# Kernel optimization log

Measured on AMD Instinct MI355X. Metric: run time of the kernel, lower is better.

Reference implementation:

```python
import jax, jax.numpy as jnp
import numpy as np

DIM = 512
N_PATCH = 1024
HEADS = 8
LN_EPS = 1e-5
NORM_EPS = 1e-12


def _layernorm(x, g, b):
    mu = jnp.mean(x, axis=-1, keepdims=True)
    var = jnp.mean(jnp.square(x - mu), axis=-1, keepdims=True)
    return (x - mu) * jax.lax.rsqrt(var + LN_EPS) * g + b


def _l2norm(x):
    # matches F.normalize(dim=-1): x / max(||x||, eps)
    n = jnp.sqrt(jnp.sum(jnp.square(x), axis=-1, keepdims=True))
    return x / jnp.maximum(n, NORM_EPS)


def _gelu(x):
    return jax.nn.gelu(x, approximate=False)


def _cosine_attn_branch(x, qkv_w, qkv_b, ln_g, ln_b, proj_w, proj_b, temperature):
    B, N, D = x.shape
    H = HEADS
    hd = D // H
    qkv = _layernorm(x @ qkv_w + qkv_b, ln_g, ln_b)          # [B,N,3D]
    q, k, v = jnp.split(qkv, 3, axis=-1)
    def to_heads(t):
        return t.reshape(B, N, H, hd).transpose(0, 2, 1, 3)  # [B,H,N,hd]
    q, k, v = to_heads(q), to_heads(k), to_heads(v)
    q = _l2norm(q)
    k = _l2norm(k)
    # temperature: [H,1,1] broadcasts over [B,H,N,N]
    attn = jnp.einsum('bhnd,bhmd->bhnm', q, k) * temperature
    attn = jax.nn.softmax(attn, axis=-1)
    out = jnp.einsum('bhnm,bhmd->bhnd', attn, v)
    out = out.transpose(0, 2, 1, 3).reshape(B, N, D)
    return out @ proj_w + proj_b


def setup_inputs() -> dict:
    key = jax.random.key(0)
    ks = iter(jax.random.split(key, 40))
    D = DIM
    def rn(shape, scale=0.02):
        return (jax.random.normal(next(ks), shape, dtype=jnp.float32) * scale)
    inp = {
        'hsi_tokens': jax.random.normal(next(ks), (8, N_PATCH, D), dtype=jnp.float32),
        'lidar_tokens': jax.random.normal(next(ks), (8, N_PATCH, D), dtype=jnp.float32),
        'temperature': jnp.ones((HEADS, 1, 1), dtype=jnp.float32),
        'sq_w': rn((D, 3 * D)), 'sq_b': jnp.zeros((3 * D,), jnp.float32),
        'sq_ln_g': jnp.ones((3 * D,), jnp.float32), 'sq_ln_b': jnp.zeros((3 * D,), jnp.float32),
        'sproj_w': rn((D, D)), 'sproj_b': jnp.zeros((D,), jnp.float32),
        'pq_w': rn((D, 3 * D)), 'pq_b': jnp.zeros((3 * D,), jnp.float32),
        'pq_ln_g': jnp.ones((3 * D,), jnp.float32), 'pq_ln_b': jnp.zeros((3 * D,), jnp.float32),
        'pproj_w': rn((D, D)), 'pproj_b': jnp.zeros((D,), jnp.float32),
        'vf_w1': rn((D, 2 * D)), 'vf_b1': jnp.zeros((2 * D,), jnp.float32),
        'vf_w2': rn((2 * D, D)), 'vf_b2': jnp.zeros((D,), jnp.float32),
        'ag_w1': rn((2 * D, D)), 'ag_b1': jnp.zeros((D,), jnp.float32),
        'ag_ln_g': jnp.ones((D,), jnp.float32), 'ag_ln_b': jnp.zeros((D,), jnp.float32),
        'ag_w2': rn((D, 3)), 'ag_b2': jnp.zeros((3,), jnp.float32),
        'fr_w1': rn((D, 2 * D)), 'fr_b1': jnp.zeros((2 * D,), jnp.float32),
        'fr_w2': rn((2 * D, D)), 'fr_b2': jnp.zeros((D,), jnp.float32),
        'alpha': jnp.ones((1,), jnp.float32),
        'beta': jnp.ones((1,), jnp.float32),
    }
    return inp


def reference(hsi_tokens, lidar_tokens, temperature,
              sq_w, sq_b, sq_ln_g, sq_ln_b, sproj_w, sproj_b,
              pq_w, pq_b, pq_ln_g, pq_ln_b, pproj_w, pproj_b,
              vf_w1, vf_b1, vf_w2, vf_b2,
              ag_w1, ag_b1, ag_ln_g, ag_ln_b, ag_w2, ag_b2,
              fr_w1, fr_b1, fr_w2, fr_b2, alpha, beta):
    B, N, D = hsi_tokens.shape
    out_spectral = _cosine_attn_branch(hsi_tokens, sq_w, sq_b, sq_ln_g, sq_ln_b,
                                       sproj_w, sproj_b, temperature)
    out_spatial = _cosine_attn_branch(lidar_tokens, pq_w, pq_b, pq_ln_g, pq_ln_b,
                                      pproj_w, pproj_b, temperature)
    # volumetric fusion MLP (dropout is identity in eval)
    s = out_spectral + out_spatial
    volumetric_feat = _gelu(s @ vf_w1 + vf_b1) @ vf_w2 + vf_b2
    # adaptive gating
    hsi_global = jnp.mean(out_spectral, axis=1)    # [B,D]
    lidar_global = jnp.mean(out_spatial, axis=1)   # [B,D]
    concat = jnp.concatenate([hsi_global, lidar_global], axis=-1)  # [B,2D]
    g = _gelu(_layernorm(concat @ ag_w1 + ag_b1, ag_ln_g, ag_ln_b))
    gate = jax.nn.softmax(g @ ag_w2 + ag_b2, axis=-1)  # [B,3]
    w_spec = gate[:, 0][:, None, None]
    w_spat = gate[:, 1][:, None, None]
    w_vol = gate[:, 2][:, None, None]
    fused = w_spec * out_spectral + w_spat * out_spatial + w_vol * volumetric_feat
    fused_recal = _gelu(fused @ fr_w1 + fr_b1) @ fr_w2 + fr_b2
    return fused + alpha * fused_recal + beta * (hsi_tokens + lidar_tokens) * 0.5
```

## Files before the change

kernel.cpp:

```cpp
#include <hip/hip_runtime.h>
#include <hip/hip_bf16.h>
#include <math.h>

#define B_   8
#define N_   1024
#define D_   512
#define H_   8
#define HD_  64
#define D3_  1536
#define M_   (B_ * N_)

#define WOFF_SQ    0
#define WOFF_PQ    786432
#define WOFF_SPROJ 1572864
#define WOFF_PPROJ 1835008
#define WOFF_VF1   2097152
#define WOFF_VF2   2621440
#define WOFF_FR1   3145728
#define WOFF_FR2   3670016

typedef float f32x4 __attribute__((ext_vector_type(4)));
typedef __bf16 bf16x8 __attribute__((ext_vector_type(8)));

union FragU {
    uint4 u4;
    unsigned int u[4];
    ushort s[8];
    bf16x8 v;
};

static __device__ __forceinline__ ushort f2bf(float x) {
    union { __bf16 h; ushort u; } c;
    c.h = (__bf16)x;
    return c.u;
}

static __device__ __forceinline__ float bf2f(ushort u) {
    union { unsigned u; float f; } c;
    c.u = ((unsigned)u) << 16;
    return c.f;
}

static __device__ __forceinline__ unsigned int pack2(float a, float b) {
    return (unsigned int)f2bf(a) | ((unsigned int)f2bf(b) << 16);
}

static __device__ __forceinline__ float gelu_f(float x) {
    return 0.5f * x * (1.0f + erff(x * 0.7071067811865475f));
}

#if __has_builtin(__builtin_amdgcn_exp2f)
static __device__ __forceinline__ float exp2_fast(float x) { return __builtin_amdgcn_exp2f(x); }
#else
static __device__ __forceinline__ float exp2_fast(float x) { return exp2f(x); }
#endif

static __device__ __forceinline__ void gload16(const ushort* g, ushort* lds) {
    __builtin_amdgcn_global_load_lds(
        (const __attribute__((address_space(1))) void*)g,
        (__attribute__((address_space(3))) void*)lds, 16, 0, 0);
}

static __device__ __forceinline__ float blk_sum(float v, float* red) {
    #pragma unroll
    for (int off = 32; off; off >>= 1) v += __shfl_xor(v, off);
    const int w = threadIdx.x >> 6;
    __syncthreads();
    if ((threadIdx.x & 63) == 0) red[w] = v;
    __syncthreads();
    return red[0] + red[1] + red[2] + red[3];
}

template <int BM, int BN, int ACT, int OUT, bool FINAL, bool GROUP>
__global__ __launch_bounds__(256) void pgemm_k(
    const ushort* __restrict__ A, const ushort* __restrict__ Wt,
    const ushort* __restrict__ Wt2, const float* __restrict__ bias,
    const float* __restrict__ bias2, int Msplit,
    void* __restrict__ Cv, int nbx, int Nn, int K,
    const ushort* __restrict__ fusedb, const float* __restrict__ r1,
    const float* __restrict__ r2, const float* __restrict__ alphap,
    const float* __restrict__ betap)
{
    constexpr int MI = BM / 32;
    constexpr int NJ = BN / 32;
    constexpr int CA = BM / 16;
    constexpr int CB = BN / 16;
    __shared__ ushort Asm[2][BM * 32];
    __shared__ ushort Bsm[2][BN * 32];
    const int tid = threadIdx.x;
    const int w = tid >> 6, l = tid & 63;
    const int cpx = gridDim.x >> 3;
    const int wg = (blockIdx.x & 7) * cpx + (blockIdx.x >> 3);
    const int m0 = (wg / nbx) * BM, n0 = (wg % nbx) * BN;
    const int wr = w >> 1, wc = w & 1;
    const int lr = l & 15, g = l >> 4;

    const ushort* W_ = (!GROUP || m0 < Msplit) ? Wt : Wt2;
    const float* b_ = (!GROUP || m0 < Msplit) ? bias : bias2;

    f32x4 acc[MI][NJ] = {};
    const int nt = K >> 5;

    #define STAGE(buf, kt)                                                        \
        do {                                                                      \
            const int k0s = (kt) << 5;                                            \
            for (int c = w; c < CA; c += 4)                                       \
                gload16(&A[(size_t)(m0 + c * 16 + lr) * K + k0s + 8 * g],         \
                        &Asm[buf][c * 512]);                                      \
            for (int c = w; c < CB; c += 4)                                       \
                gload16(&W_[(size_t)(n0 + c * 16 + lr) * K + k0s + 8 * g],        \
                        &Bsm[buf][c * 512]);                                      \
        } while (0)

    STAGE(0, 0);
    __syncthreads();
    int cur = 0;
    for (int t = 0; t < nt; ++t) {
        if (t + 1 < nt) STAGE(cur ^ 1, t + 1);
        FragU af[MI], bf4[NJ];
        #pragma unroll
        for (int mi = 0; mi < MI; ++mi)
            af[mi].u4 = *reinterpret_cast<const uint4*>(
                &Asm[cur][(wr * MI + mi) * 512 + l * 8]);
        #pragma unroll
        for (int nj = 0; nj < NJ; ++nj)
            bf4[nj].u4 = *reinterpret_cast<const uint4*>(
                &Bsm[cur][(wc * NJ + nj) * 512 + l * 8]);
        #pragma unroll
        for (int mi = 0; mi < MI; ++mi)
            #pragma unroll
            for (int nj = 0; nj < NJ; ++nj)
                acc[mi][nj] = __builtin_amdgcn_mfma_f32_16x16x32_bf16(
                    af[mi].v, bf4[nj].v, acc[mi][nj], 0, 0, 0);
        __syncthreads();
        cur ^= 1;
    }
    #undef STAGE

    float alpha = 0.f, beta = 0.f;
    if (FINAL) { alpha = alphap[0]; beta = betap[0]; }
    #pragma unroll
    for (int mi = 0; mi < MI; ++mi) {
        #pragma unroll
        for (int r = 0; r < 4; ++r) {
            const int m = m0 + wr * (MI * 16) + mi * 16 + g * 4 + r;
            #pragma unroll
            for (int nj = 0; nj < NJ; ++nj) {
                const int n = n0 + wc * (NJ * 16) + nj * 16 + lr;
                const size_t idx = (size_t)m * Nn + n;
                float v = acc[mi][nj][r] + b_[n];
                if (ACT == 1) v = gelu_f(v);
                if (FINAL)
                    v = bf2f(fusedb[idx]) + alpha * v + 0.5f * beta * (r1[idx] + r2[idx]);
                if (OUT == 0) ((float*)Cv)[idx] = v;
                else          ((ushort*)Cv)[idx] = f2bf(v);
            }
        }
    }
}

__global__ __launch_bounds__(256) void cvtw_k(
    const float* __restrict__ w0, const float* __restrict__ w1,
    const float* __restrict__ w2, const float* __restrict__ w3,
    const float* __restrict__ w4, const float* __restrict__ w5,
    const float* __restrict__ w6, const float* __restrict__ w7,
    ushort* __restrict__ dst)
{
    __shared__ ushort T[64][72];
    const int id = blockIdx.z;
    int K, Nn, off;
    const float* src;
    switch (id) {
        case 0: src = w0; K = 512;  Nn = 1536; off = WOFF_SQ;    break;
        case 1: src = w1; K = 512;  Nn = 1536; off = WOFF_PQ;    break;
        case 2: src = w2; K = 512;  Nn = 512;  off = WOFF_SPROJ; break;
        case 3: src = w3; K = 512;  Nn = 512;  off = WOFF_PPROJ; break;
        case 4: src = w4; K = 512;  Nn = 1024; off = WOFF_VF1;   break;
        case 5: src = w5; K = 1024; Nn = 512;  off = WOFF_VF2;   break;
        case 6: src = w6; K = 512;  Nn = 1024; off = WOFF_FR1;   break;
        default: src = w7; K = 1024; Nn = 512; off = WOFF_FR2;   break;
    }
    const int n0 = blockIdx.x * 64, k0 = blockIdx.y * 64;
    if (n0 >= Nn || k0 >= K) return;
    const int t = threadIdx.x;
    const int q = t >> 6, e = t & 63;
    #pragma unroll 4
    for (int i = 0; i < 16; ++i) {
        const int kl = q * 16 + i;
        T[e][kl] = f2bf(src[(size_t)(k0 + kl) * Nn + n0 + e]);
    }
    __syncthreads();
    #pragma unroll 4
    for (int i = 0; i < 16; ++i) {
        const int nl = q * 16 + i;
        dst[(size_t)off + (size_t)(n0 + nl) * K + k0 + e] = T[nl][e];
    }
}

__global__ __launch_bounds__(256) void cvt_k(const float* __restrict__ a,
                                             ushort* __restrict__ dst)
{
    const size_t i = ((size_t)blockIdx.x * 256 + threadIdx.x) * 8;
    const float4 x0 = *reinterpret_cast<const float4*>(a + i);
    const float4 x1 = *reinterpret_cast<const float4*>(a + i + 4);
    FragU o;
    o.u[0] = pack2(x0.x, x0.y);
    o.u[1] = pack2(x0.z, x0.w);
    o.u[2] = pack2(x1.x, x1.y);
    o.u[3] = pack2(x1.z, x1.w);
    *reinterpret_cast<uint4*>(dst + i) = o.u4;
}

__global__ __launch_bounds__(256) void cvtadd_k(const ushort* __restrict__ a,
                                                const ushort* __restrict__ b,
                                                ushort* __restrict__ dst)
{
    const size_t i = ((size_t)blockIdx.x * 256 + threadIdx.x) * 8;
    FragU x, y, o;
    x.u4 = *reinterpret_cast<const uint4*>(a + i);
    y.u4 = *reinterpret_cast<const uint4*>(b + i);
    #pragma unroll
    for (int e = 0; e < 8; ++e) o.s[e] = f2bf(bf2f(x.s[e]) + bf2f(y.s[e]));
    *reinterpret_cast<uint4*>(dst + i) = o.u4;
}

__global__ __launch_bounds__(256) void lnprep_k(ushort* __restrict__ x,
                                                const float* __restrict__ lng0,
                                                const float* __restrict__ lnb0,
                                                const float* __restrict__ lng1,
                                                const float* __restrict__ lnb1,
                                                const float* __restrict__ temp,
                                                ushort* __restrict__ Kb,
                                                ushort* __restrict__ Vt)
{
    __shared__ ushort Vs[8 * 512];
    const int w = threadIdx.x >> 6, l = threadIdx.x & 63;
    const int n0 = blockIdx.x * 8;
    const float L2E = 1.4426950408889634f;
    const float* lng = (n0 < 8192) ? lng0 : lng1;
    const float* lnb = (n0 < 8192) ? lnb0 : lnb1;

    #pragma unroll
    for (int rr = 0; rr < 2; ++rr) {
        const int row = n0 + w * 2 + rr;
        const int bb = row >> 10;
        const int n = row & 1023;
        ushort* xr = x + (size_t)row * D3_;
        float qv[24];
        #pragma unroll
        for (int i = 0; i < 24; ++i) qv[i] = bf2f(xr[l + 64 * i]);
        float s = 0.f, ss = 0.f;
        #pragma unroll
        for (int i = 0; i < 24; ++i) { s += qv[i]; ss += qv[i] * qv[i]; }
        #pragma unroll
        for (int off = 32; off; off >>= 1) {
            s += __shfl_xor(s, off);
            ss += __shfl_xor(ss, off);
        }
        const float mu = s * (1.0f / D3_);
        const float var = ss * (1.0f / D3_) - mu * mu;
        const float rs = rsqrtf(var + 1e-5f);
        #pragma unroll
        for (int i = 0; i < 24; ++i)
            qv[i] = (qv[i] - mu) * rs * lng[l + 64 * i] + lnb[l + 64 * i];
        float sq[16];
        #pragma unroll
        for (int i = 0; i < 16; ++i) sq[i] = qv[i] * qv[i];
        #pragma unroll
        for (int off = 32; off; off >>= 1)
            #pragma unroll
            for (int i = 0; i < 16; ++i) sq[i] += __shfl_xor(sq[i], off);
        #pragma unroll
        for (int i = 0; i < 8; ++i) {
            const float qs = temp[i] * L2E / fmaxf(sqrtf(sq[i]), 1e-12f);
            xr[i * 64 + l] = f2bf(qv[i] * qs);
        }
        #pragma unroll
        for (int i = 0; i < 8; ++i) {
            const float ks = 1.0f / fmaxf(sqrtf(sq[8 + i]), 1e-12f);
            Kb[((size_t)(bb * 8 + i) * N_ + n) * HD_ + l] = f2bf(qv[8 + i] * ks);
        }
        #pragma unroll
        for (int i = 0; i < 8; ++i)
            Vs[(w * 2 + rr) * 512 + i * 64 + l] = f2bf(qv[16 + i]);
    }
    __syncthreads();
    const int bb = n0 >> 10;
    #pragma unroll
    for (int it = 0; it < 2; ++it) {
        const int combo = threadIdx.x + it * 256;
        FragU f;
        #pragma unroll
        for (int tok = 0; tok < 8; ++tok) f.s[tok] = Vs[tok * 512 + combo];
        *reinterpret_cast<uint4*>(
            &Vt[((size_t)(bb * 8 + (combo >> 6)) * HD_ + (combo & 63)) * N_ + (n0 & 1023)]) = f.u4;
    }
}

__global__ __launch_bounds__(256) void fattn_k(const ushort* __restrict__ Qu,
                                               const ushort* __restrict__ Kb,
                                               const ushort* __restrict__ Vt,
                                               const float* __restrict__ temp,
                                               ushort* __restrict__ out)
{
    __shared__ ushort Ks[64 * 72];
    __shared__ ushort Vs[64 * 72];
    const int tid = threadIdx.x;
    const int cpx = gridDim.x >> 3;
    const int wg = (blockIdx.x & 7) * cpx + (blockIdx.x >> 3);
    const int nb = wg & 7;
    const int h  = (wg >> 3) & 7;
    const int bb = wg >> 6;
    const int bh = bb * 8 + h;
    const int n0 = nb * 128;
    const int w  = tid >> 6;
    const int l  = tid & 63;
    const int lr = l & 15;
    const int g  = l >> 4;
    const float m2 = fabsf(temp[h]) * 1.4426950408889634f;

    const int qb = n0 + w * 32;
    FragU qa0, qa1, qb0, qb1;
    {
        const size_t rb0 = (size_t)(bb * N_ + qb + lr) * D3_ + h * 64 + 8 * g;
        const size_t rb1 = (size_t)(bb * N_ + qb + 16 + lr) * D3_ + h * 64 + 8 * g;
        qa0.u4 = *reinterpret_cast<const uint4*>(&Qu[rb0]);
        qa1.u4 = *reinterpret_cast<const uint4*>(&Qu[rb0 + 32]);
        qb0.u4 = *reinterpret_cast<const uint4*>(&Qu[rb1]);
        qb1.u4 = *reinterpret_cast<const uint4*>(&Qu[rb1 + 32]);
    }

    f32x4 OA[4] = {};
    f32x4 OB[4] = {};
    float lsA = 0.f, lsB = 0.f;

    const ushort* kbase = Kb + (size_t)bh * N_ * HD_;
    const ushort* vbase = Vt + (size_t)bh * HD_ * N_;
    const int sr = tid >> 3;
    const int sc = (tid & 7) * 8;
    uint4 k0r, k1r, v0r, v1r;

    #define LOADT(kt)                                                           \
        do {                                                                    \
            const ushort* ks_ = kbase + (size_t)((kt) * 64) * HD_;              \
            const ushort* vs_ = vbase + (kt) * 64;                              \
            k0r = *reinterpret_cast<const uint4*>(ks_ + sr * HD_ + sc);         \
            k1r = *reinterpret_cast<const uint4*>(ks_ + (sr + 32) * HD_ + sc);  \
            v0r = *reinterpret_cast<const uint4*>(vs_ + (size_t)sr * N_ + sc);  \
            v1r = *reinterpret_cast<const uint4*>(vs_ + (size_t)(sr + 32) * N_ + sc); \
        } while (0)
    #define WRITET()                                                            \
        do {                                                                    \
            *reinterpret_cast<uint4*>(&Ks[sr * 72 + sc]) = k0r;                 \
            *reinterpret_cast<uint4*>(&Ks[(sr + 32) * 72 + sc]) = k1r;          \
            *reinterpret_cast<uint4*>(&Vs[sr * 72 + sc]) = v0r;                 \
            *reinterpret_cast<uint4*>(&Vs[(sr + 32) * 72 + sc]) = v1r;          \
        } while (0)

    LOADT(0);
    WRITET();
    __syncthreads();

    #pragma unroll 1
    for (int kt = 0; kt < 16; ++kt) {
        if (kt < 15) LOADT(kt + 1);

        unsigned paA[2][4], paB[2][4];
        #pragma unroll
        for (int j = 0; j < 4; ++j) {
            FragU ka, kc;
            ka.u4 = *reinterpret_cast<const uint4*>(&Ks[(j * 16 + lr) * 72 + 8 * g]);
            kc.u4 = *reinterpret_cast<const uint4*>(&Ks[(j * 16 + lr) * 72 + 32 + 8 * g]);
            f32x4 sA = {0.f,0.f,0.f,0.f}, sB = {0.f,0.f,0.f,0.f};
            sA = __builtin_amdgcn_mfma_f32_16x16x32_bf16(ka.v, qa0.v, sA, 0, 0, 0);
            sA = __builtin_amdgcn_mfma_f32_16x16x32_bf16(kc.v, qa1.v, sA, 0, 0, 0);
            sB = __builtin_amdgcn_mfma_f32_16x16x32_bf16(ka.v, qb0.v, sB, 0, 0, 0);
            sB = __builtin_amdgcn_mfma_f32_16x16x32_bf16(kc.v, qb1.v, sB, 0, 0, 0);
            float pA[4], pB[4];
            #pragma unroll
            for (int r = 0; r < 4; ++r) {
                pA[r] = exp2_fast(sA[r] - m2);
                pB[r] = exp2_fast(sB[r] - m2);
                lsA += pA[r];
                lsB += pB[r];
            }
            paA[j >> 1][2 * (j & 1) + 0] = pack2(pA[0], pA[1]);
            paA[j >> 1][2 * (j & 1) + 1] = pack2(pA[2], pA[3]);
            paB[j >> 1][2 * (j & 1) + 0] = pack2(pB[0], pB[1]);
            paB[j >> 1][2 * (j & 1) + 1] = pack2(pB[2], pB[3]);
        }

        #pragma unroll
        for (int ks = 0; ks < 2; ++ks) {
            FragU fa, fb2;
            fa.u[0] = paA[ks][0]; fa.u[1] = paA[ks][1];
            fa.u[2] = paA[ks][2]; fa.u[3] = paA[ks][3];
            fb2.u[0] = paB[ks][0]; fb2.u[1] = paB[ks][1];
            fb2.u[2] = paB[ks][2]; fb2.u[3] = paB[ks][3];
            #pragma unroll
            for (int s4 = 0; s4 < 4; ++s4) {
                FragU vb;
                const int vi = (lr + 16 * s4) * 72 + ks * 32 + 4 * g;
                *reinterpret_cast<uint2*>(&vb.u[0]) =
                    *reinterpret_cast<const uint2*>(&Vs[vi]);
                *reinterpret_cast<uint2*>(&vb.u[2]) =
                    *reinterpret_cast<const uint2*>(&Vs[vi + 16]);
                OA[s4] = __builtin_amdgcn_mfma_f32_16x16x32_bf16(fa.v, vb.v, OA[s4], 0, 0, 0);
                OB[s4] = __builtin_amdgcn_mfma_f32_16x16x32_bf16(fb2.v, vb.v, OB[s4], 0, 0, 0);
            }
        }

        if (kt < 15) {
            __syncthreads();
            WRITET();
            __syncthreads();
        }
    }
    #undef LOADT
    #undef WRITET

    lsA += __shfl_xor(lsA, 16); lsA += __shfl_xor(lsA, 32);
    lsB += __shfl_xor(lsB, 16); lsB += __shfl_xor(lsB, 32);
    const float invA = 1.0f / lsA;
    const float invB = 1.0f / lsB;
    ushort* outp = out + ((size_t)(bb * N_) + qb) * D_ + h * HD_;
    #pragma unroll
    for (int r = 0; r < 4; ++r) {
        const float iA = __shfl(invA, 4 * g + r);
        const float iB = __shfl(invB, 4 * g + r);
        ushort* rowA = outp + (size_t)(4 * g + r) * D_;
        ushort* rowB = outp + (size_t)(16 + 4 * g + r) * D_;
        #pragma unroll
        for (int s4 = 0; s4 < 4; ++s4) {
            rowA[s4 * 16 + lr] = f2bf(OA[s4][r] * iA);
            rowB[s4 * 16 + lr] = f2bf(OB[s4][r] * iB);
        }
    }
}

__global__ __launch_bounds__(256) void means_k(const ushort* __restrict__ spec,
                                               const ushort* __restrict__ spat,
                                               float* __restrict__ Gp)
{
    const int b = blockIdx.x >> 5;
    const int ch = blockIdx.x & 31;
    const int n0 = ch * 32;
    const int d0 = threadIdx.x * 2;
    float s1a = 0.f, s1b = 0.f, s2a = 0.f, s2b = 0.f;
    #pragma unroll 4
    for (int n = 0; n < 32; ++n) {
        const size_t idx = ((size_t)(b * N_) + n0 + n) * D_ + d0;
        ushort u1[2], u2[2];
        *reinterpret_cast<unsigned*>(u1) = *reinterpret_cast<const unsigned*>(spec + idx);
        *reinterpret_cast<unsigned*>(u2) = *reinterpret_cast<const unsigned*>(spat + idx);
        s1a += bf2f(u1[0]); s1b += bf2f(u1[1]);
        s2a += bf2f(u2[0]); s2b += bf2f(u2[1]);
    }
    float* gp = Gp + (size_t)blockIdx.x * 1024;
    gp[d0] = s1a; gp[d0 + 1] = s1b;
    gp[512 + d0] = s2a; gp[512 + d0 + 1] = s2b;
}

__global__ __launch_bounds__(256) void gate1_k(const float* __restrict__ Gp,
                                               const float* __restrict__ w1,
                                               const float* __restrict__ b1,
                                               float* __restrict__ y)
{
    __shared__ float xs[1024];
    __shared__ float red[4][64];
    const int jc = blockIdx.x, b = blockIdx.y, tid = threadIdx.x;
    for (int k = tid; k < 1024; k += 256) {
        float s = 0.f;
        #pragma unroll 8
        for (int c = 0; c < 32; ++c) s += Gp[(size_t)(b * 32 + c) * 1024 + k];
        xs[k] = s * (1.0f / N_);
    }
    __syncthreads();
    const int jl = tid & 63;
    const int jj = jc * 64 + jl;
    const int seg = tid >> 6;
    float acc = 0.f;
    const float* wp = w1 + (size_t)(seg * 256) * 512 + jj;
    const float* xp = xs + seg * 256;
    #pragma unroll 8
    for (int k = 0; k < 256; ++k) acc += xp[k] * wp[(size_t)k * 512];
    red[seg][jl] = acc;
    __syncthreads();
    if (tid < 64)
        y[b * 512 + jc * 64 + tid] =
            red[0][tid] + red[1][tid] + red[2][tid] + red[3][tid] + b1[jc * 64 + tid];
}

__global__ __launch_bounds__(256) void gate2_k(const float* __restrict__ y,
                                               const float* __restrict__ lng,
                                               const float* __restrict__ lnb,
                                               const float* __restrict__ w2,
                                               const float* __restrict__ b2,
                                               float* __restrict__ gate)
{
    __shared__ float red[4];
    const int b = blockIdx.x, tid = threadIdx.x;
    const float v0 = y[b * 512 + tid];
    const float v1 = y[b * 512 + 256 + tid];
    const float s = blk_sum(v0 + v1, red);
    const float ss = blk_sum(v0 * v0 + v1 * v1, red);
    const float mu = s * (1.0f / 512.0f);
    const float var = ss * (1.0f / 512.0f) - mu * mu;
    const float rs = rsqrtf(var + 1e-5f);
    const float z0 = gelu_f((v0 - mu) * rs * lng[tid] + lnb[tid]);
    const float z1 = gelu_f((v1 - mu) * rs * lng[tid + 256] + lnb[tid + 256]);
    float p0 = z0 * w2[tid * 3 + 0] + z1 * w2[(tid + 256) * 3 + 0];
    float p1 = z0 * w2[tid * 3 + 1] + z1 * w2[(tid + 256) * 3 + 1];
    float p2 = z0 * w2[tid * 3 + 2] + z1 * w2[(tid + 256) * 3 + 2];
    p0 = blk_sum(p0, red);
    p1 = blk_sum(p1, red);
    p2 = blk_sum(p2, red);
    if (tid == 0) {
        p0 += b2[0]; p1 += b2[1]; p2 += b2[2];
        const float m = fmaxf(p0, fmaxf(p1, p2));
        const float e0 = expf(p0 - m), e1 = expf(p1 - m), e2 = expf(p2 - m);
        const float inv = 1.0f / (e0 + e1 + e2);
        gate[b * 3 + 0] = e0 * inv;
        gate[b * 3 + 1] = e1 * inv;
        gate[b * 3 + 2] = e2 * inv;
    }
}

__global__ __launch_bounds__(256) void fuse_k(
    const ushort* __restrict__ spec, const ushort* __restrict__ spat,
    const ushort* __restrict__ volb, const float* __restrict__ gate,
    ushort* __restrict__ fb)
{
    const size_t i4 = ((size_t)blockIdx.x * 256 + threadIdx.x) * 4;
    const int b = (int)(i4 >> 19);
    const float g0 = gate[b * 3 + 0], g1 = gate[b * 3 + 1], g2 = gate[b * 3 + 2];
    ushort au[4], cu[4], vu[4];
    *reinterpret_cast<uint2*>(au) = *reinterpret_cast<const uint2*>(spec + i4);
    *reinterpret_cast<uint2*>(cu) = *reinterpret_cast<const uint2*>(spat + i4);
    *reinterpret_cast<uint2*>(vu) = *reinterpret_cast<const uint2*>(volb + i4);
    union { ushort s[4]; uint2 u; } ob;
    #pragma unroll
    for (int e = 0; e < 4; ++e)
        ob.s[e] = f2bf(g0 * bf2f(au[e]) + g1 * bf2f(cu[e]) + g2 * bf2f(vu[e]));
    *reinterpret_cast<uint2*>(fb + i4) = ob.u;
}

extern "C" void kernel_launch(void* const* d_in, const int* in_sizes, int n_in,
                              void* d_out, int out_size, void* d_ws, size_t ws_size,
                              hipStream_t stream)
{
    const float* hsi    = (const float*)d_in[0];
    const float* lidar  = (const float*)d_in[1];
    const float* temp   = (const float*)d_in[2];
    const float* sq_w   = (const float*)d_in[3];
    const float* sq_b   = (const float*)d_in[4];
    const float* sq_lng = (const float*)d_in[5];
    const float* sq_lnb = (const float*)d_in[6];
    const float* sproj_w = (const float*)d_in[7];
    const float* sproj_b = (const float*)d_in[8];
    const float* pq_w   = (const float*)d_in[9];
    const float* pq_b   = (const float*)d_in[10];
    const float* pq_lng = (const float*)d_in[11];
    const float* pq_lnb = (const float*)d_in[12];
    const float* pproj_w = (const float*)d_in[13];
    const float* pproj_b = (const float*)d_in[14];
    const float* vf_w1  = (const float*)d_in[15];
    const float* vf_b1  = (const float*)d_in[16];
    const float* vf_w2  = (const float*)d_in[17];
    const float* vf_b2  = (const float*)d_in[18];
    const float* ag_w1  = (const float*)d_in[19];
    const float* ag_b1  = (const float*)d_in[20];
    const float* ag_lng = (const float*)d_in[21];
    const float* ag_lnb = (const float*)d_in[22];
    const float* ag_w2  = (const float*)d_in[23];
    const float* ag_b2  = (const float*)d_in[24];
    const float* fr_w1  = (const float*)d_in[25];
    const float* fr_b1  = (const float*)d_in[26];
    const float* fr_w2  = (const float*)d_in[27];
    const float* fr_b2  = (const float*)d_in[28];
    const float* alpha  = (const float*)d_in[29];
    const float* beta   = (const float*)d_in[30];
    float* out = (float*)d_out;

    ushort* base = (ushort*)d_ws;
    ushort* Qkv  = base;
    ushort* Ob   = base;
    ushort* Sb   = base + 8388608;
    ushort* volb = base + 12582912;
    ushort* fb   = base + 16777216;
    float*  Gp   = (float*)(base + 20971520);
    float*  gate = Gp + 262144;
    float*  ybuf = gate + 64;
    ushort* Kb   = base + 25165824;
    ushort* Vt   = base + 33554432;
    ushort* Hb   = base + 25165824;
    ushort* Ab   = base + 41943040;
    ushort* Xb   = base + 41943040;
    ushort* Wb   = base + 50331648;

    const dim3 blk(256);

    cvtw_k<<<dim3(24, 16, 8), blk, 0, stream>>>(sq_w, pq_w, sproj_w, pproj_w,
                                                vf_w1, vf_w2, fr_w1, fr_w2, Wb);
    cvt_k<<<2048, blk, 0, stream>>>(hsi, Xb);
    cvt_k<<<2048, blk, 0, stream>>>(lidar, Xb + (size_t)M_ * D_);

    pgemm_k<128,128,0,1,false,true><<<1536, blk, 0, stream>>>(
        Xb, Wb + WOFF_SQ, Wb + WOFF_PQ, sq_b, pq_b, M_,
        Qkv, 12, D3_, D_, nullptr, nullptr, nullptr, nullptr, nullptr);

    lnprep_k<<<2048, blk, 0, stream>>>(Qkv, sq_lng, sq_lnb, pq_lng, pq_lnb,
                                       temp, Kb, Vt);

    fattn_k<<<1024, blk, 0, stream>>>(Qkv, Kb, Vt, temp, Ab);

    pgemm_k<128,64,0,1,false,true><<<1024, blk, 0, stream>>>(
        Ab, Wb + WOFF_SPROJ, Wb + WOFF_PPROJ, sproj_b, pproj_b, M_,
        Ob, 8, D_, D_, nullptr, nullptr, nullptr, nullptr, nullptr);

    const ushort* spec_b = Ob;
    const ushort* spat_b = Ob + (size_t)M_ * D_;

    means_k<<<256, blk, 0, stream>>>(spec_b, spat_b, Gp);
    gate1_k<<<dim3(8, 8), blk, 0, stream>>>(Gp, ag_w1, ag_b1, ybuf);
    gate2_k<<<B_, blk, 0, stream>>>(ybuf, ag_lng, ag_lnb, ag_w2, ag_b2, gate);

    cvtadd_k<<<2048, blk, 0, stream>>>(spec_b, spat_b, Sb);
    pgemm_k<128,64,1,1,false,false><<<1024, blk, 0, stream>>>(
        Sb, Wb + WOFF_VF1, nullptr, vf_b1, nullptr, 0,
        Hb, 16, 1024, D_, nullptr, nullptr, nullptr, nullptr, nullptr);
    pgemm_k<128,64,0,1,false,false><<<512, blk, 0, stream>>>(
        Hb, Wb + WOFF_VF2, nullptr, vf_b2, nullptr, 0,
        volb, 8, D_, 1024, nullptr, nullptr, nullptr, nullptr, nullptr);

    fuse_k<<<4096, blk, 0, stream>>>(spec_b, spat_b, volb, gate, fb);
    pgemm_k<128,64,1,1,false,false><<<1024, blk, 0, stream>>>(
        fb, Wb + WOFF_FR1, nullptr, fr_b1, nullptr, 0,
        Hb, 16, 1024, D_, nullptr, nullptr, nullptr, nullptr, nullptr);
    pgemm_k<128,64,0,0,true,false><<<512, blk, 0, stream>>>(
        Hb, Wb + WOFF_FR2, nullptr, fr_b2, nullptr, 0,
        out, 8, D_, 1024, fb, hsi, lidar, alpha, beta);
}
```

Measured before the change: 355.3 us.

## Fuse input conversions with bf16 residual and move softmax sums onto MFMA

Merges the two input conversion kernels into one that also writes a bf16 half-sum residual, so the final GEMM epilogue reads one bf16 array instead of two fp32 inputs. In flash attention, the max offset is folded into the MFMA accumulator init, row sums are computed with an MFMA against a ones vector instead of scalar adds and shuffles, and V shared-memory stores and loads are XOR-swizzled to reduce bank conflicts. The residual now carries bf16 rounding, and the row sums use the bf16-rounded probabilities rather than the fp32 values.

```diff
diff --git a/kernel.cpp b/kernel.cpp
--- a/kernel.cpp
+++ b/kernel.cpp
@@ -77,9 +77,8 @@
     const ushort* __restrict__ Wt2, const float* __restrict__ bias,
     const float* __restrict__ bias2, int Msplit,
     void* __restrict__ Cv, int nbx, int Nn, int K,
-    const ushort* __restrict__ fusedb, const float* __restrict__ r1,
-    const float* __restrict__ r2, const float* __restrict__ alphap,
-    const float* __restrict__ betap)
+    const ushort* __restrict__ fusedb, const ushort* __restrict__ resb,
+    const float* __restrict__ alphap, const float* __restrict__ betap)
 {
     constexpr int MI = BM / 32;
     constexpr int NJ = BN / 32;
@@ -151,7 +150,7 @@
                 float v = acc[mi][nj][r] + b_[n];
                 if (ACT == 1) v = gelu_f(v);
                 if (FINAL)
-                    v = bf2f(fusedb[idx]) + alpha * v + 0.5f * beta * (r1[idx] + r2[idx]);
+                    v = bf2f(fusedb[idx]) + alpha * v + beta * bf2f(resb[idx]);
                 if (OUT == 0) ((float*)Cv)[idx] = v;
                 else          ((ushort*)Cv)[idx] = f2bf(v);
             }
@@ -197,18 +196,29 @@
     }
 }
 
-__global__ __launch_bounds__(256) void cvt_k(const float* __restrict__ a,
-                                             ushort* __restrict__ dst)
+__global__ __launch_bounds__(256) void cvt3_k(const float* __restrict__ h,
+                                              const float* __restrict__ l,
+                                              ushort* __restrict__ xh,
+                                              ushort* __restrict__ xl,
+                                              ushort* __restrict__ rb)
 {
     const size_t i = ((size_t)blockIdx.x * 256 + threadIdx.x) * 8;
-    const float4 x0 = *reinterpret_cast<const float4*>(a + i);
-    const float4 x1 = *reinterpret_cast<const float4*>(a + i + 4);
-    FragU o;
-    o.u[0] = pack2(x0.x, x0.y);
-    o.u[1] = pack2(x0.z, x0.w);
-    o.u[2] = pack2(x1.x, x1.y);
-    o.u[3] = pack2(x1.z, x1.w);
-    *reinterpret_cast<uint4*>(dst + i) = o.u4;
+    const float4 h0 = *reinterpret_cast<const float4*>(h + i);
+    const float4 h1 = *reinterpret_cast<const float4*>(h + i + 4);
+    const float4 l0 = *reinterpret_cast<const float4*>(l + i);
+    const float4 l1 = *reinterpret_cast<const float4*>(l + i + 4);
+    FragU oh, ol, orr;
+    oh.u[0] = pack2(h0.x, h0.y); oh.u[1] = pack2(h0.z, h0.w);
+    oh.u[2] = pack2(h1.x, h1.y); oh.u[3] = pack2(h1.z, h1.w);
+    ol.u[0] = pack2(l0.x, l0.y); ol.u[1] = pack2(l0.z, l0.w);
+    ol.u[2] = pack2(l1.x, l1.y); ol.u[3] = pack2(l1.z, l1.w);
+    orr.u[0] = pack2(0.5f * (h0.x + l0.x), 0.5f * (h0.y + l0.y));
+    orr.u[1] = pack2(0.5f * (h0.z + l0.z), 0.5f * (h0.w + l0.w));
+    orr.u[2] = pack2(0.5f * (h1.x + l1.x), 0.5f * (h1.y + l1.y));
+    orr.u[3] = pack2(0.5f * (h1.z + l1.z), 0.5f * (h1.w + l1.w));
+    *reinterpret_cast<uint4*>(xh + i) = oh.u4;
+    *reinterpret_cast<uint4*>(xl + i) = ol.u4;
+    *reinterpret_cast<uint4*>(rb + i) = orr.u4;
 }
 
 __global__ __launch_bounds__(256) void cvtadd_k(const ushort* __restrict__ a,
@@ -318,6 +328,10 @@
     const int lr = l & 15;
     const int g  = l >> 4;
     const float m2 = fabsf(temp[h]) * 1.4426950408889634f;
+    const f32x4 mInit = {-m2, -m2, -m2, -m2};
+
+    FragU ones;
+    ones.u[0] = ones.u[1] = ones.u[2] = ones.u[3] = 0x3F803F80u;
 
     const int qb = n0 + w * 32;
     FragU qa0, qa1, qb0, qb1;
@@ -332,12 +346,14 @@
 
     f32x4 OA[4] = {};
     f32x4 OB[4] = {};
-    float lsA = 0.f, lsB = 0.f;
+    f32x4 LSA = {0.f, 0.f, 0.f, 0.f};
+    f32x4 LSB = {0.f, 0.f, 0.f, 0.f};
 
     const ushort* kbase = Kb + (size_t)bh * N_ * HD_;
     const ushort* vbase = Vt + (size_t)bh * HD_ * N_;
     const int sr = tid >> 3;
     const int sc = (tid & 7) * 8;
+    const int scv = sc ^ (8 * (sr & 1));
     uint4 k0r, k1r, v0r, v1r;
 
     #define LOADT(kt)                                                           \
@@ -353,8 +369,8 @@
         do {                                                                    \
             *reinterpret_cast<uint4*>(&Ks[sr * 72 + sc]) = k0r;                 \
             *reinterpret_cast<uint4*>(&Ks[(sr + 32) * 72 + sc]) = k1r;          \
-            *reinterpret_cast<uint4*>(&Vs[sr * 72 + sc]) = v0r;                 \
-            *reinterpret_cast<uint4*>(&Vs[(sr + 32) * 72 + sc]) = v1r;          \
+            *reinterpret_cast<uint4*>(&Vs[sr * 72 + scv]) = v0r;                \
+            *reinterpret_cast<uint4*>(&Vs[(sr + 32) * 72 + scv]) = v1r;         \
         } while (0)
 
     LOADT(0);
@@ -371,7 +387,7 @@
             FragU ka, kc;
             ka.u4 = *reinterpret_cast<const uint4*>(&Ks[(j * 16 + lr) * 72 + 8 * g]);
             kc.u4 = *reinterpret_cast<const uint4*>(&Ks[(j * 16 + lr) * 72 + 32 + 8 * g]);
-            f32x4 sA = {0.f,0.f,0.f,0.f}, sB = {0.f,0.f,0.f,0.f};
+            f32x4 sA = mInit, sB = mInit;
             sA = __builtin_amdgcn_mfma_f32_16x16x32_bf16(ka.v, qa0.v, sA, 0, 0, 0);
             sA = __builtin_amdgcn_mfma_f32_16x16x32_bf16(kc.v, qa1.v, sA, 0, 0, 0);
             sB = __builtin_amdgcn_mfma_f32_16x16x32_bf16(ka.v, qb0.v, sB, 0, 0, 0);
@@ -379,10 +395,8 @@
             float pA[4], pB[4];
             #pragma unroll
             for (int r = 0; r < 4; ++r) {
-                pA[r] = exp2_fast(sA[r] - m2);
-                pB[r] = exp2_fast(sB[r] - m2);
-                lsA += pA[r];
-                lsB += pB[r];
+                pA[r] = exp2_fast(sA[r]);
+                pB[r] = exp2_fast(sB[r]);
             }
             paA[j >> 1][2 * (j & 1) + 0] = pack2(pA[0], pA[1]);
             paA[j >> 1][2 * (j & 1) + 1] = pack2(pA[2], pA[3]);
@@ -397,10 +411,12 @@
             fa.u[2] = paA[ks][2]; fa.u[3] = paA[ks][3];
             fb2.u[0] = paB[ks][0]; fb2.u[1] = paB[ks][1];
             fb2.u[2] = paB[ks][2]; fb2.u[3] = paB[ks][3];
+            LSA = __builtin_amdgcn_mfma_f32_16x16x32_bf16(fa.v, ones.v, LSA, 0, 0, 0);
+            LSB = __builtin_amdgcn_mfma_f32_16x16x32_bf16(fb2.v, ones.v, LSB, 0, 0, 0);
             #pragma unroll
             for (int s4 = 0; s4 < 4; ++s4) {
                 FragU vb;
-                const int vi = (lr + 16 * s4) * 72 + ks * 32 + 4 * g;
+                const int vi = (lr + 16 * s4) * 72 + ((ks * 32 + 4 * g) ^ (8 * (lr & 1)));
                 *reinterpret_cast<uint2*>(&vb.u[0]) =
                     *reinterpret_cast<const uint2*>(&Vs[vi]);
                 *reinterpret_cast<uint2*>(&vb.u[2]) =
@@ -419,15 +435,11 @@
     #undef LOADT
     #undef WRITET
 
-    lsA += __shfl_xor(lsA, 16); lsA += __shfl_xor(lsA, 32);
-    lsB += __shfl_xor(lsB, 16); lsB += __shfl_xor(lsB, 32);
-    const float invA = 1.0f / lsA;
-    const float invB = 1.0f / lsB;
     ushort* outp = out + ((size_t)(bb * N_) + qb) * D_ + h * HD_;
     #pragma unroll
     for (int r = 0; r < 4; ++r) {
-        const float iA = __shfl(invA, 4 * g + r);
-        const float iB = __shfl(invB, 4 * g + r);
+        const float iA = 1.0f / LSA[r];
+        const float iB = 1.0f / LSB[r];
         ushort* rowA = outp + (size_t)(4 * g + r) * D_;
         ushort* rowB = outp + (size_t)(16 + 4 * g + r) * D_;
         #pragma unroll
@@ -597,17 +609,17 @@
     ushort* Ab   = base + 41943040;
     ushort* Xb   = base + 41943040;
     ushort* Wb   = base + 50331648;
+    ushort* Rb   = base + 54525952;
 
     const dim3 blk(256);
 
     cvtw_k<<<dim3(24, 16, 8), blk, 0, stream>>>(sq_w, pq_w, sproj_w, pproj_w,
                                                 vf_w1, vf_w2, fr_w1, fr_w2, Wb);
-    cvt_k<<<2048, blk, 0, stream>>>(hsi, Xb);
-    cvt_k<<<2048, blk, 0, stream>>>(lidar, Xb + (size_t)M_ * D_);
+    cvt3_k<<<2048, blk, 0, stream>>>(hsi, lidar, Xb, Xb + (size_t)M_ * D_, Rb);
 
     pgemm_k<128,128,0,1,false,true><<<1536, blk, 0, stream>>>(
         Xb, Wb + WOFF_SQ, Wb + WOFF_PQ, sq_b, pq_b, M_,
-        Qkv, 12, D3_, D_, nullptr, nullptr, nullptr, nullptr, nullptr);
+        Qkv, 12, D3_, D_, nullptr, nullptr, nullptr, nullptr);
 
     lnprep_k<<<2048, blk, 0, stream>>>(Qkv, sq_lng, sq_lnb, pq_lng, pq_lnb,
                                        temp, Kb, Vt);
@@ -616,7 +628,7 @@
 
     pgemm_k<128,64,0,1,false,true><<<1024, blk, 0, stream>>>(
         Ab, Wb + WOFF_SPROJ, Wb + WOFF_PPROJ, sproj_b, pproj_b, M_,
-        Ob, 8, D_, D_, nullptr, nullptr, nullptr, nullptr, nullptr);
+        Ob, 8, D_, D_, nullptr, nullptr, nullptr, nullptr);
 
     const ushort* spec_b = Ob;
     const ushort* spat_b = Ob + (size_t)M_ * D_;
@@ -628,16 +640,16 @@
     cvtadd_k<<<2048, blk, 0, stream>>>(spec_b, spat_b, Sb);
     pgemm_k<128,64,1,1,false,false><<<1024, blk, 0, stream>>>(
         Sb, Wb + WOFF_VF1, nullptr, vf_b1, nullptr, 0,
-        Hb, 16, 1024, D_, nullptr, nullptr, nullptr, nullptr, nullptr);
+        Hb, 16, 1024, D_, nullptr, nullptr, nullptr, nullptr);
     pgemm_k<128,64,0,1,false,false><<<512, blk, 0, stream>>>(
         Hb, Wb + WOFF_VF2, nullptr, vf_b2, nullptr, 0,
-        volb, 8, D_, 1024, nullptr, nullptr, nullptr, nullptr, nullptr);
+        volb, 8, D_, 1024, nullptr, nullptr, nullptr, nullptr);
 
     fuse_k<<<4096, blk, 0, stream>>>(spec_b, spat_b, volb, gate, fb);
     pgemm_k<128,64,1,1,false,false><<<1024, blk, 0, stream>>>(
         fb, Wb + WOFF_FR1, nullptr, fr_b1, nullptr, 0,
-        Hb, 16, 1024, D_, nullptr, nullptr, nullptr, nullptr, nullptr);
+        Hb, 16, 1024, D_, nullptr, nullptr, nullptr, nullptr);
     pgemm_k<128,64,0,0,true,false><<<512, blk, 0, stream>>>(
         Hb, Wb + WOFF_FR2, nullptr, fr_b2, nullptr, 0,
-        out, 8, D_, 1024, fb, hsi, lidar, alpha, beta);
-}
+        out, 8, D_, 1024, fb, Rb, alpha, beta);
+}
```

Result: no change. 355.3 us (+0.0%).
